# Kernel optimization log

Measured on AMD Instinct MI355X. Metric: run time of the kernel, lower is better.

The kernel has to match this reference:

```python
import jax, jax.numpy as jnp
import numpy as np

B, S, D = 1, 2048, 2048
HQ, HKV = 32, 8
HD = D // HQ          # 64
G = HQ // HKV         # 4 query heads per kv head


def apply_rope(x, freq):
    # x: (b, h, s, hd); freq: (s, hd//2) angles. Llama-style pairwise rotation.
    cos = jnp.cos(freq)  # (s, hd//2)
    sin = jnp.sin(freq)
    xr = x.reshape(*x.shape[:-1], HD // 2, 2)
    xe, xo = xr[..., 0], xr[..., 1]
    re = xe * cos - xo * sin
    ro = xe * sin + xo * cos
    return jnp.stack([re, ro], axis=-1).reshape(x.shape)


def setup_inputs() -> dict:
    key = jax.random.key(0)
    k1, k2, k3, k4, k5 = jax.random.split(key, 5)
    x = jax.random.normal(k1, (B, S, D), dtype=jnp.float32)
    # RoPE angles: pos * inv_freq, theta=10000
    inv_freq = 1.0 / (10000.0 ** (jnp.arange(0, HD, 2, dtype=jnp.float32) / HD))
    freq = jnp.arange(S, dtype=jnp.float32)[:, None] * inv_freq[None, :]  # (S, HD//2)
    mask = jnp.tril(jnp.ones((S, S), dtype=jnp.int32))
    scale = D ** -0.5
    wq = jax.random.normal(k2, (D, HQ * HD), dtype=jnp.float32) * scale
    wk = jax.random.normal(k3, (D, HKV * HD), dtype=jnp.float32) * scale
    wv = jax.random.normal(k4, (D, HKV * HD), dtype=jnp.float32) * scale
    wo = jax.random.normal(k5, (HQ * HD, D), dtype=jnp.float32) * scale
    return {"x": x, "freq": freq, "mask": mask, "wq": wq, "wk": wk, "wv": wv, "wo": wo}


def reference(x, freq, mask, wq, wk, wv, wo):
    b, s, d = x.shape
    q = (x @ wq).reshape(b, s, HQ, HD).transpose(0, 2, 1, 3)    # (b,HQ,s,hd)
    k = (x @ wk).reshape(b, s, HKV, HD).transpose(0, 2, 1, 3)   # (b,HKV,s,hd)
    v = (x @ wv).reshape(b, s, HKV, HD).transpose(0, 2, 1, 3)
    q = apply_rope(q, freq[:s])
    k = apply_rope(k, freq[:s])
    # GQA: broadcast kv heads over groups instead of repeat_interleave
    qg = q.reshape(b, HKV, G, s, HD)
    scores = jnp.einsum('bhgsd,bhtd->bhgst', qg, k)             # (b,HKV,G,s,s)
    scores = jnp.where(mask[:s, :s] == 0, -jnp.inf, scores)
    w = jax.nn.softmax(scores * (HD ** -0.5), axis=-1)
    out = jnp.einsum('bhgst,bhtd->bhgsd', w, v)
    out = out.reshape(b, HQ, s, HD).transpose(0, 2, 1, 3).reshape(b, s, HQ * HD)
    return out @ wo
```

## Files before the change

### kernel.cpp

```cpp
#include <hip/hip_runtime.h>

typedef unsigned short u16;
typedef unsigned int u32;
typedef unsigned long long u64;

using bf16x8 = __bf16 __attribute__((ext_vector_type(8)));
using f32x4  = float  __attribute__((ext_vector_type(4)));

#define LDS_SPACE __attribute__((address_space(3)))
#define GLB_SPACE __attribute__((address_space(1)))

static __device__ __forceinline__ u16 f2bf(float f) {
  union { float f; u32 u; } c; c.f = f;
  u32 u = c.u;
  return (u16)((u + 0x7fffu + ((u >> 16) & 1u)) >> 16);
}
static __device__ __forceinline__ float bf2f(u16 u) {
  union { u32 u; float f; } c; c.u = ((u32)u) << 16;
  return c.f;
}

static __device__ __forceinline__ void fence_barrier() {
  asm volatile("" ::: "memory");
  __builtin_amdgcn_s_barrier();
  asm volatile("" ::: "memory");
}

__global__ __launch_bounds__(256) void cvt_f32_bf16_k(const float* __restrict__ src,
                                                      u16* __restrict__ dst, int n4) {
  int i = blockIdx.x * 256 + threadIdx.x;
  if (i >= n4) return;
  float4 v = ((const float4*)src)[i];
  ushort4 o;
  o.x = f2bf(v.x); o.y = f2bf(v.y); o.z = f2bf(v.z); o.w = f2bf(v.w);
  ((ushort4*)dst)[i] = o;
}

__global__ __launch_bounds__(256) void transpose_cvt_k(const float* __restrict__ src,
                                                       u16* __restrict__ dst, int R, int C) {
  __shared__ float t[32][33];
  int lx = threadIdx.x & 31, ly = threadIdx.x >> 5;
  int r0 = blockIdx.y * 32, c0 = blockIdx.x * 32;
  #pragma unroll
  for (int i = 0; i < 32; i += 8)
    t[ly + i][lx] = src[(size_t)(r0 + ly + i) * C + c0 + lx];
  __syncthreads();
  #pragma unroll
  for (int i = 0; i < 32; i += 8)
    dst[(size_t)(c0 + ly + i) * R + r0 + lx] = f2bf(t[lx][ly + i]);
}

__global__ __launch_bounds__(256) void vtrans_k(const u16* __restrict__ Y,
                                                u16* __restrict__ Vt) {
  __shared__ u16 t[64][72];
  const int s0 = blockIdx.x * 64;
  const int c0 = blockIdx.y * 64;
  const int lx = threadIdx.x & 63, ly = threadIdx.x >> 6;
  #pragma unroll
  for (int i = 0; i < 64; i += 4)
    t[i + ly][lx] = Y[(size_t)(s0 + i + ly) * 3072 + 2560 + c0 + lx];
  __syncthreads();
  #pragma unroll
  for (int i = 0; i < 64; i += 4)
    Vt[(size_t)(c0 + i + ly) * 2048 + s0 + lx] = t[lx][i + ly];
}

template <typename OutT>
__global__ __launch_bounds__(256) void gemm64_k(const u16* __restrict__ A,
                                                const u16* __restrict__ Bt,
                                                OutT* __restrict__ C,
                                                int M, int N, int K) {
  __shared__ u16 As[2][64 * 64];
  __shared__ u16 Bs[2][128 * 64];
  const int tid = threadIdx.x, lane = tid & 63, w = tid >> 6;
  const int wr = w >> 1, wc = w & 1;
  const int bm = blockIdx.y, bn = blockIdx.x;
  const int l15 = lane & 15, lq = lane >> 4;
  f32x4 acc[2][4] = {};

  const int srow8 = lane >> 3;
  const int scolb = ((lane & 7) ^ srow8) * 16;
  const u16* AgR = A + (size_t)(bm * 64 + w * 16 + srow8) * K;
  const u16* BgR = Bt + (size_t)(bn * 128 + w * 32 + srow8) * K;

  auto stage = [&](int buf, int k0) {
    #pragma unroll
    for (int i = 0; i < 2; ++i)
      __builtin_amdgcn_global_load_lds(
          (const GLB_SPACE u32*)((const char*)(AgR + (size_t)i * 8 * K + k0) + scolb),
          (LDS_SPACE u32*)&As[buf][(w * 16 + i * 8) * 64], 16, 0, 0);
    #pragma unroll
    for (int i = 0; i < 4; ++i)
      __builtin_amdgcn_global_load_lds(
          (const GLB_SPACE u32*)((const char*)(BgR + (size_t)i * 8 * K + k0) + scolb),
          (LDS_SPACE u32*)&Bs[buf][(w * 32 + i * 8) * 64], 16, 0, 0);
  };

  stage(0, 0);
  for (int k0 = 0; k0 < K; k0 += 64) {
    const int cur = (k0 >> 6) & 1;
    fence_barrier();
    if (k0 + 64 < K) {
      stage(cur ^ 1, k0 + 64);
      asm volatile("s_waitcnt vmcnt(6)" ::: "memory");
    } else {
      asm volatile("s_waitcnt vmcnt(0)" ::: "memory");
    }
    fence_barrier();

    #pragma unroll
    for (int kk = 0; kk < 2; ++kk) {
      bf16x8 a[2], b[4];
      #pragma unroll
      for (int m = 0; m < 2; ++m) {
        const int ra = wr * 32 + m * 16 + l15;
        a[m] = *(const bf16x8*)&As[cur][ra * 64 + (((kk * 4 + lq) ^ (ra & 7)) << 3)];
      }
      #pragma unroll
      for (int n = 0; n < 4; ++n) {
        const int rb = wc * 64 + n * 16 + l15;
        b[n] = *(const bf16x8*)&Bs[cur][rb * 64 + (((kk * 4 + lq) ^ (rb & 7)) << 3)];
      }
      #pragma unroll
      for (int m = 0; m < 2; ++m)
        #pragma unroll
        for (int n = 0; n < 4; ++n)
          acc[m][n] = __builtin_amdgcn_mfma_f32_16x16x32_bf16(a[m], b[n], acc[m][n], 0, 0, 0);
    }
  }

  const int r0 = bm * 64 + wr * 32 + lq * 4;
  const int c0 = bn * 128 + wc * 64 + l15;
  #pragma unroll
  for (int m = 0; m < 2; ++m)
    #pragma unroll
    for (int n = 0; n < 4; ++n)
      #pragma unroll
      for (int r = 0; r < 4; ++r) {
        float v = acc[m][n][r];
        size_t off = (size_t)(r0 + m * 16 + r) * N + (c0 + n * 16);
        if constexpr (sizeof(OutT) == 2) ((u16*)C)[off] = f2bf(v);
        else C[off] = v;
      }
}

__global__ __launch_bounds__(256) void rope_k(u16* __restrict__ Y,
                                              const float* __restrict__ freq) {
  int idx = blockIdx.x * 256 + threadIdx.x;
  int s = idx / 1280;
  int rem = idx - s * 1280;
  int h = rem >> 5;
  int i = rem & 31;
  int col = (h < 32) ? (h * 64 + 2 * i) : (2048 + (h - 32) * 64 + 2 * i);
  float ang = freq[s * 32 + i];
  float sn, cs;
  sincosf(ang, &sn, &cs);
  size_t base = (size_t)s * 3072 + col;
  float e = bf2f(Y[base]), o = bf2f(Y[base + 1]);
  Y[base]     = f2bf(e * cs - o * sn);
  Y[base + 1] = f2bf(e * sn + o * cs);
}

constexpr float SC = 0.18033688011112042f;

__global__ __launch_bounds__(256, 3) void attn_part_k(const u16* __restrict__ Y,
                                                      const u16* __restrict__ Vtg,
                                                      u16* __restrict__ Opart,
                                                      float2* __restrict__ Ml,
                                                      u16* __restrict__ Out) {
  __shared__ u16 Ks[2][64 * 64];
  __shared__ u16 Vs[2][64 * 64];
  __shared__ u32 Ps[4][2][16 * 36];
  const int w = threadIdx.x >> 6, lane = threadIdx.x & 63;
  const int l15 = lane & 15, lq = lane >> 4;

  const int b = (int)blockIdx.x;
  const int head = b & 31;
  const int idx = b >> 5;
  const u64 tb = (idx < 12) ? 986161012810415591ULL : 1200400570313029ULL;
  const int v = (int)((tb >> ((idx < 12 ? idx : idx - 12) * 5)) & 31);
  const int qt = v & 15, ch = v >> 4;
  const int kvh = head >> 2;
  const int ntiles = 2 * qt + 2;
  const int half = qt + 1;
  const int tstart = ch ? half : 0;
  const int tend = (qt >= 8 && ch == 0) ? half : ntiles;
  const int q0w = qt * 128 + w * 32;

  const int srow = lane >> 3;
  const int scolb = ((lane & 7) ^ srow) * 16;
  auto stage = [&](int buf, int t) {
    const int t0 = t * 64;
    #pragma unroll
    for (int i = 0; i < 2; ++i) {
      const int r = w * 16 + i * 8;
      const char* gk = (const char*)(Y + (size_t)(t0 + r + srow) * 3072 + 2048 + kvh * 64) + scolb;
      __builtin_amdgcn_global_load_lds((const GLB_SPACE u32*)gk,
                                       (LDS_SPACE u32*)&Ks[buf][r * 64], 16, 0, 0);
      const char* gv = (const char*)(Vtg + (size_t)(kvh * 64 + r + srow) * 2048 + t0) + scolb;
      __builtin_amdgcn_global_load_lds((const GLB_SPACE u32*)gv,
                                       (LDS_SPACE u32*)&Vs[buf][r * 64], 16, 0, 0);
    }
  };

  stage(0, tstart);

  bf16x8 qf[2][2];
  #pragma unroll
  for (int qs = 0; qs < 2; ++qs)
    #pragma unroll
    for (int kk = 0; kk < 2; ++kk)
      qf[qs][kk] = *(const bf16x8*)&Y[(size_t)(q0w + qs * 16 + l15) * 3072 +
                                      head * 64 + kk * 32 + lq * 8];

  float m_[2] = { -1e30f, -1e30f };
  float l_[2] = { 0.f, 0.f };
  f32x4 accO[2][4] = {};

  for (int t = tstart; t < tend; ++t) {
    const int cur = (t - tstart) & 1;
    fence_barrier();
    if (t + 1 < tend) {
      stage(cur ^ 1, t + 1);
      asm volatile("s_waitcnt vmcnt(4)" ::: "memory");
    } else {
      asm volatile("s_waitcnt vmcnt(0)" ::: "memory");
    }
    fence_barrier();

    const int t0 = t * 64;
    if (t0 > q0w + 31) continue;

    const u16* Kb = Ks[cur];
    const u16* Vb = Vs[cur];

    f32x4 sc[2][4] = {};
    #pragma unroll
    for (int kk = 0; kk < 2; ++kk)
      #pragma unroll
      for (int kt = 0; kt < 4; ++kt) {
        const int rk = kt * 16 + l15;
        bf16x8 a = *(const bf16x8*)&Kb[rk * 64 + ((((kk * 4 + lq) ^ (rk & 7)) << 3))];
        sc[0][kt] = __builtin_amdgcn_mfma_f32_16x16x32_bf16(a, qf[0][kk], sc[0][kt], 0, 0, 0);
        sc[1][kt] = __builtin_amdgcn_mfma_f32_16x16x32_bf16(a, qf[1][kk], sc[1][kt], 0, 0, 0);
      }

    bool act[2];
    #pragma unroll
    for (int qs = 0; qs < 2; ++qs) {
      const int qsmin = q0w + qs * 16;
      act[qs] = (t0 <= qsmin + 15);
      if (!act[qs]) continue;
      const int qrow = qsmin + l15;
      if (t0 + 63 > qsmin) {
        #pragma unroll
        for (int n = 0; n < 4; ++n)
          #pragma unroll
          for (int rr = 0; rr < 4; ++rr)
            if (t0 + n * 16 + lq * 4 + rr > qrow) sc[qs][n][rr] = -1e30f;
      }
      float a0 = fmaxf(fmaxf(sc[qs][0][0], sc[qs][0][1]), fmaxf(sc[qs][0][2], sc[qs][0][3]));
      float a1 = fmaxf(fmaxf(sc[qs][1][0], sc[qs][1][1]), fmaxf(sc[qs][1][2], sc[qs][1][3]));
      float a2 = fmaxf(fmaxf(sc[qs][2][0], sc[qs][2][1]), fmaxf(sc[qs][2][2], sc[qs][2][3]));
      float a3 = fmaxf(fmaxf(sc[qs][3][0], sc[qs][3][1]), fmaxf(sc[qs][3][2], sc[qs][3][3]));
      float mx = fmaxf(fmaxf(a0, a1), fmaxf(a2, a3));

      if (__any(mx > m_[qs] + 40.0f)) {
        float mf = mx;
        mf = fmaxf(mf, __shfl_xor(mf, 16));
        mf = fmaxf(mf, __shfl_xor(mf, 32));
        const float mnew = fmaxf(m_[qs], mf);
        const float alpha = exp2f((m_[qs] - mnew) * SC);
        l_[qs] *= alpha;
        #pragma unroll
        for (int dt = 0; dt < 4; ++dt) accO[qs][dt] *= alpha;
        m_[qs] = mnew;
      }
      const float mS = m_[qs] * SC;
      float s0 = 0.f, s1 = 0.f, s2 = 0.f, s3 = 0.f;
      u64* pp = (u64*)&Ps[w][qs][l15 * 36 + lq * 2];
      #pragma unroll
      for (int n = 0; n < 4; ++n) {
        float p0 = exp2f(sc[qs][n][0] * SC - mS);
        float p1 = exp2f(sc[qs][n][1] * SC - mS);
        float p2 = exp2f(sc[qs][n][2] * SC - mS);
        float p3 = exp2f(sc[qs][n][3] * SC - mS);
        s0 += p0; s1 += p1; s2 += p2; s3 += p3;
        u32 w0, w1;
        asm("v_cvt_pk_bf16_f32 %0, %1, %2" : "=v"(w0) : "v"(p0), "v"(p1));
        asm("v_cvt_pk_bf16_f32 %0, %1, %2" : "=v"(w1) : "v"(p2), "v"(p3));
        pp[n * 4] = (u64)w0 | ((u64)w1 << 32);
      }
      l_[qs] += (s0 + s1) + (s2 + s3);
    }

    #pragma unroll
    for (int qs = 0; qs < 2; ++qs) {
      if (!act[qs]) continue;
      const u16* p16 = (const u16*)Ps[w][qs];
      #pragma unroll
      for (int c = 0; c < 2; ++c) {
        bf16x8 bb = *(const bf16x8*)&p16[l15 * 72 + c * 32 + lq * 8];
        #pragma unroll
        for (int dt = 0; dt < 4; ++dt) {
          const int rv = dt * 16 + l15;
          bf16x8 vfr = *(const bf16x8*)&Vb[rv * 64 + ((((c * 4 + lq) ^ (rv & 7)) << 3))];
          accO[qs][dt] = __builtin_amdgcn_mfma_f32_16x16x32_bf16(vfr, bb, accO[qs][dt], 0, 0, 0);
        }
      }
    }
  }

  if (qt < 8) {
    #pragma unroll
    for (int qs = 0; qs < 2; ++qs) {
      float lt = l_[qs];
      lt += __shfl_xor(lt, 16);
      lt += __shfl_xor(lt, 32);
      const float rl = 1.0f / lt;
      const int qrow = q0w + qs * 16 + l15;
      #pragma unroll
      for (int dt = 0; dt < 4; ++dt) {
        ushort4 o;
        o.x = f2bf(accO[qs][dt][0] * rl);
        o.y = f2bf(accO[qs][dt][1] * rl);
        o.z = f2bf(accO[qs][dt][2] * rl);
        o.w = f2bf(accO[qs][dt][3] * rl);
        *(ushort4*)&Out[(size_t)qrow * 2048 + head * 64 + dt * 16 + lq * 4] = o;
      }
    }
    return;
  }

  const int slot = ((head << 3) + (qt - 8)) * 2 + ch;
  u16* ob = Opart + (size_t)slot * 8192;
  #pragma unroll
  for (int qs = 0; qs < 2; ++qs) {
    float lt = l_[qs];
    lt += __shfl_xor(lt, 16);
    lt += __shfl_xor(lt, 32);
    const int row = w * 32 + qs * 16 + l15;
    #pragma unroll
    for (int dt = 0; dt < 4; ++dt) {
      ushort4 o;
      o.x = f2bf(accO[qs][dt][0]);
      o.y = f2bf(accO[qs][dt][1]);
      o.z = f2bf(accO[qs][dt][2]);
      o.w = f2bf(accO[qs][dt][3]);
      *(ushort4*)&ob[row * 64 + dt * 16 + lq * 4] = o;
    }
    if (lq == 0) Ml[(size_t)slot * 128 + row] = make_float2(m_[qs], lt);
  }
}

__global__ __launch_bounds__(256) void attn_comb_k(const u16* __restrict__ Opart,
                                                   const float2* __restrict__ Ml,
                                                   u16* __restrict__ Out) {
  const int b = blockIdx.x;
  const int rg = b & 3;
  const int hq = b >> 2;
  const int head = hq >> 3;
  const int qt8 = hq & 7;
  const int slot0 = ((head << 3) + qt8) * 2;
  const int rl = threadIdx.x >> 3;
  const int d8 = (threadIdx.x & 7) * 8;
  const int row = rg * 32 + rl;

  float2 ml0 = Ml[(size_t)slot0 * 128 + row];
  float2 ml1 = Ml[(size_t)(slot0 + 1) * 128 + row];
  const float gm = fmaxf(ml0.x, ml1.x);
  const float a0 = exp2f((ml0.x - gm) * SC);
  const float a1 = exp2f((ml1.x - gm) * SC);
  const float rd = 1.0f / (a0 * ml0.y + a1 * ml1.y);

  const u16* p0 = &Opart[(size_t)slot0 * 8192 + row * 64 + d8];
  const u16* p1 = &Opart[(size_t)(slot0 + 1) * 8192 + row * 64 + d8];
  ushort4 q0 = *(const ushort4*)p0, q1 = *(const ushort4*)(p0 + 4);
  ushort4 r0 = *(const ushort4*)p1, r1 = *(const ushort4*)(p1 + 4);
  ushort4 o0, o1;
  o0.x = f2bf((a0 * bf2f(q0.x) + a1 * bf2f(r0.x)) * rd);
  o0.y = f2bf((a0 * bf2f(q0.y) + a1 * bf2f(r0.y)) * rd);
  o0.z = f2bf((a0 * bf2f(q0.z) + a1 * bf2f(r0.z)) * rd);
  o0.w = f2bf((a0 * bf2f(q0.w) + a1 * bf2f(r0.w)) * rd);
  o1.x = f2bf((a0 * bf2f(q1.x) + a1 * bf2f(r1.x)) * rd);
  o1.y = f2bf((a0 * bf2f(q1.y) + a1 * bf2f(r1.y)) * rd);
  o1.z = f2bf((a0 * bf2f(q1.z) + a1 * bf2f(r1.z)) * rd);
  o1.w = f2bf((a0 * bf2f(q1.w) + a1 * bf2f(r1.w)) * rd);
  u16* op = &Out[(size_t)((qt8 + 8) * 128 + row) * 2048 + head * 64 + d8];
  *(ushort4*)op = o0;
  *(ushort4*)(op + 4) = o1;
}

extern "C" void kernel_launch(void* const* d_in, const int* in_sizes, int n_in,
                              void* d_out, int out_size, void* d_ws, size_t ws_size,
                              hipStream_t stream) {
  const float* x    = (const float*)d_in[0];
  const float* freq = (const float*)d_in[1];
  const float* wq   = (const float*)d_in[3];
  const float* wk   = (const float*)d_in[4];
  const float* wv   = (const float*)d_in[5];
  const float* wo   = (const float*)d_in[6];
  float* out = (float*)d_out;

  u16* x_bf   = (u16*)d_ws;
  u16* wqkv_t = x_bf + (size_t)2048 * 2048;
  u16* wo_t   = wqkv_t + (size_t)3072 * 2048;
  u16* y      = wo_t + (size_t)2048 * 2048;
  u16* attn   = y + (size_t)2048 * 3072;
  u16* vt     = x_bf;
  u16* opart  = attn + (size_t)2048 * 2048;
  float2* ml  = (float2*)(opart + (size_t)512 * 8192);

  cvt_f32_bf16_k<<<4096, 256, 0, stream>>>(x, x_bf, 2048 * 2048 / 4);
  transpose_cvt_k<<<dim3(64, 64), 256, 0, stream>>>(wq, wqkv_t, 2048, 2048);
  transpose_cvt_k<<<dim3(16, 64), 256, 0, stream>>>(wk, wqkv_t + (size_t)2048 * 2048, 2048, 512);
  transpose_cvt_k<<<dim3(16, 64), 256, 0, stream>>>(wv, wqkv_t + (size_t)2560 * 2048, 2048, 512);
  transpose_cvt_k<<<dim3(64, 64), 256, 0, stream>>>(wo, wo_t, 2048, 2048);

  gemm64_k<u16><<<dim3(24, 32), 256, 0, stream>>>(x_bf, wqkv_t, y, 2048, 3072, 2048);
  rope_k<<<10240, 256, 0, stream>>>(y, freq);
  vtrans_k<<<dim3(32, 8), 256, 0, stream>>>(y, vt);
  attn_part_k<<<768, 256, 0, stream>>>(y, vt, opart, ml, attn);
  attn_comb_k<<<1024, 256, 0, stream>>>(opart, ml, attn);
  gemm64_k<float><<<dim3(16, 32), 256, 0, stream>>>(attn, wo_t, out, 2048, 2048, 2048);
}
```

Measured before the change: 144.5 us.

## Merge prep kernels, fold softmax scale into Wq, hoist V fragment loads

Result: faster. 135.4 us (-6.3%).

```diff
diff --git a/kernel.cpp b/kernel.cpp
--- a/kernel.cpp
+++ b/kernel.cpp
@@ -26,28 +26,40 @@
   asm volatile("" ::: "memory");
 }
 
-__global__ __launch_bounds__(256) void cvt_f32_bf16_k(const float* __restrict__ src,
-                                                      u16* __restrict__ dst, int n4) {
-  int i = blockIdx.x * 256 + threadIdx.x;
-  if (i >= n4) return;
-  float4 v = ((const float4*)src)[i];
-  ushort4 o;
-  o.x = f2bf(v.x); o.y = f2bf(v.y); o.z = f2bf(v.z); o.w = f2bf(v.w);
-  ((ushort4*)dst)[i] = o;
-}
-
-__global__ __launch_bounds__(256) void transpose_cvt_k(const float* __restrict__ src,
-                                                       u16* __restrict__ dst, int R, int C) {
+constexpr float SC = 0.18033688011112042f;
+
+__global__ __launch_bounds__(256) void prep_k(const float* __restrict__ x,
+                                              const float* __restrict__ wq,
+                                              const float* __restrict__ wk,
+                                              const float* __restrict__ wv,
+                                              const float* __restrict__ wo,
+                                              u16* __restrict__ x_bf,
+                                              u16* __restrict__ wqkv_t,
+                                              u16* __restrict__ wo_t) {
+  const int b = blockIdx.x;
+  if (b < 4096) {
+    int i = b * 256 + threadIdx.x;
+    float4 v = ((const float4*)x)[i];
+    ushort4 o;
+    o.x = f2bf(v.x); o.y = f2bf(v.y); o.z = f2bf(v.z); o.w = f2bf(v.w);
+    ((ushort4*)x_bf)[i] = o;
+    return;
+  }
+  const float* src; u16* dst; int C, bx, by; float scale = 1.0f;
+  if (b < 8192)      { src = wq; dst = wqkv_t; C = 2048; int t = b - 4096; bx = t & 63; by = t >> 6; scale = SC; }
+  else if (b < 9216) { src = wk; dst = wqkv_t + (size_t)2048 * 2048; C = 512; int t = b - 8192; bx = t & 15; by = t >> 4; }
+  else if (b < 10240){ src = wv; dst = wqkv_t + (size_t)2560 * 2048; C = 512; int t = b - 9216; bx = t & 15; by = t >> 4; }
+  else               { src = wo; dst = wo_t; C = 2048; int t = b - 10240; bx = t & 63; by = t >> 6; }
   __shared__ float t[32][33];
-  int lx = threadIdx.x & 31, ly = threadIdx.x >> 5;
-  int r0 = blockIdx.y * 32, c0 = blockIdx.x * 32;
+  const int lx = threadIdx.x & 31, ly = threadIdx.x >> 5;
+  const int r0 = by * 32, c0 = bx * 32;
   #pragma unroll
   for (int i = 0; i < 32; i += 8)
     t[ly + i][lx] = src[(size_t)(r0 + ly + i) * C + c0 + lx];
   __syncthreads();
   #pragma unroll
   for (int i = 0; i < 32; i += 8)
-    dst[(size_t)(c0 + ly + i) * R + r0 + lx] = f2bf(t[lx][ly + i]);
+    dst[(size_t)(c0 + ly + i) * 2048 + r0 + lx] = f2bf(t[lx][ly + i] * scale);
 }
 
 __global__ __launch_bounds__(256) void vtrans_k(const u16* __restrict__ Y,
@@ -161,8 +173,6 @@
   Y[base + 1] = f2bf(e * sn + o * cs);
 }
 
-constexpr float SC = 0.18033688011112042f;
-
 __global__ __launch_bounds__(256, 3) void attn_part_k(const u16* __restrict__ Y,
                                                       const u16* __restrict__ Vtg,
                                                       u16* __restrict__ Opart,
@@ -245,6 +255,15 @@
         sc[1][kt] = __builtin_amdgcn_mfma_f32_16x16x32_bf16(a, qf[1][kk], sc[1][kt], 0, 0, 0);
       }
 
+    bf16x8 vf[2][4];
+    #pragma unroll
+    for (int c = 0; c < 2; ++c)
+      #pragma unroll
+      for (int dt = 0; dt < 4; ++dt) {
+        const int rv = dt * 16 + l15;
+        vf[c][dt] = *(const bf16x8*)&Vb[rv * 64 + ((((c * 4 + lq) ^ (rv & 7)) << 3))];
+      }
+
     bool act[2];
     #pragma unroll
     for (int qs = 0; qs < 2; ++qs) {
@@ -265,26 +284,26 @@
       float a3 = fmaxf(fmaxf(sc[qs][3][0], sc[qs][3][1]), fmaxf(sc[qs][3][2], sc[qs][3][3]));
       float mx = fmaxf(fmaxf(a0, a1), fmaxf(a2, a3));
 
-      if (__any(mx > m_[qs] + 40.0f)) {
+      if (__any(mx > m_[qs] + 7.25f)) {
         float mf = mx;
         mf = fmaxf(mf, __shfl_xor(mf, 16));
         mf = fmaxf(mf, __shfl_xor(mf, 32));
         const float mnew = fmaxf(m_[qs], mf);
-        const float alpha = exp2f((m_[qs] - mnew) * SC);
+        const float alpha = exp2f(m_[qs] - mnew);
         l_[qs] *= alpha;
         #pragma unroll
         for (int dt = 0; dt < 4; ++dt) accO[qs][dt] *= alpha;
         m_[qs] = mnew;
       }
-      const float mS = m_[qs] * SC;
+      const float mS = m_[qs];
       float s0 = 0.f, s1 = 0.f, s2 = 0.f, s3 = 0.f;
       u64* pp = (u64*)&Ps[w][qs][l15 * 36 + lq * 2];
       #pragma unroll
       for (int n = 0; n < 4; ++n) {
-        float p0 = exp2f(sc[qs][n][0] * SC - mS);
-        float p1 = exp2f(sc[qs][n][1] * SC - mS);
-        float p2 = exp2f(sc[qs][n][2] * SC - mS);
-        float p3 = exp2f(sc[qs][n][3] * SC - mS);
+        float p0 = exp2f(sc[qs][n][0] - mS);
+        float p1 = exp2f(sc[qs][n][1] - mS);
+        float p2 = exp2f(sc[qs][n][2] - mS);
+        float p3 = exp2f(sc[qs][n][3] - mS);
         s0 += p0; s1 += p1; s2 += p2; s3 += p3;
         u32 w0, w1;
         asm("v_cvt_pk_bf16_f32 %0, %1, %2" : "=v"(w0) : "v"(p0), "v"(p1));
@@ -302,11 +321,8 @@
       for (int c = 0; c < 2; ++c) {
         bf16x8 bb = *(const bf16x8*)&p16[l15 * 72 + c * 32 + lq * 8];
         #pragma unroll
-        for (int dt = 0; dt < 4; ++dt) {
-          const int rv = dt * 16 + l15;
-          bf16x8 vfr = *(const bf16x8*)&Vb[rv * 64 + ((((c * 4 + lq) ^ (rv & 7)) << 3))];
-          accO[qs][dt] = __builtin_amdgcn_mfma_f32_16x16x32_bf16(vfr, bb, accO[qs][dt], 0, 0, 0);
-        }
+        for (int dt = 0; dt < 4; ++dt)
+          accO[qs][dt] = __builtin_amdgcn_mfma_f32_16x16x32_bf16(vf[c][dt], bb, accO[qs][dt], 0, 0, 0);
       }
     }
   }
@@ -369,8 +385,8 @@
   float2 ml0 = Ml[(size_t)slot0 * 128 + row];
   float2 ml1 = Ml[(size_t)(slot0 + 1) * 128 + row];
   const float gm = fmaxf(ml0.x, ml1.x);
-  const float a0 = exp2f((ml0.x - gm) * SC);
-  const float a1 = exp2f((ml1.x - gm) * SC);
+  const float a0 = exp2f(ml0.x - gm);
+  const float a1 = exp2f(ml1.x - gm);
   const float rd = 1.0f / (a0 * ml0.y + a1 * ml1.y);
 
   const u16* p0 = &Opart[(size_t)slot0 * 8192 + row * 64 + d8];
@@ -411,12 +427,7 @@
   u16* opart  = attn + (size_t)2048 * 2048;
   float2* ml  = (float2*)(opart + (size_t)512 * 8192);
 
-  cvt_f32_bf16_k<<<4096, 256, 0, stream>>>(x, x_bf, 2048 * 2048 / 4);
-  transpose_cvt_k<<<dim3(64, 64), 256, 0, stream>>>(wq, wqkv_t, 2048, 2048);
-  transpose_cvt_k<<<dim3(16, 64), 256, 0, stream>>>(wk, wqkv_t + (size_t)2048 * 2048, 2048, 512);
-  transpose_cvt_k<<<dim3(16, 64), 256, 0, stream>>>(wv, wqkv_t + (size_t)2560 * 2048, 2048, 512);
-  transpose_cvt_k<<<dim3(64, 64), 256, 0, stream>>>(wo, wo_t, 2048, 2048);
-
+  prep_k<<<14336, 256, 0, stream>>>(x, wq, wk, wv, wo, x_bf, wqkv_t, wo_t);
   gemm64_k<u16><<<dim3(24, 32), 256, 0, stream>>>(x_bf, wqkv_t, y, 2048, 3072, 2048);
   rope_k<<<10240, 256, 0, stream>>>(y, freq);
   vtrans_k<<<dim3(32, 8), 256, 0, stream>>>(y, vt);
```
